# Optimization experiments

Measured on AMD Instinct MI355X. Metric: run time of the kernel, lower is better.

Reference implementation:

```python
import jax, jax.numpy as jnp
import numpy as np

CLAMP = 15  # relative positions clipped to [-15, 15], shifted to [0, 30]


def setup_inputs() -> dict:
    key = jax.random.key(0)
    ks = jax.random.split(key, 8)
    B, L, C, P = 2, 512, 256, 128
    return {
        "single_repr": jax.random.normal(ks[0], (B, L, C), jnp.float32),
        "pair_bias": jax.random.normal(ks[1], (B, L, L, 2), jnp.float32),
        "mask": jax.random.uniform(ks[2], (B, L), jnp.float32),
        "w_outer": jax.random.normal(ks[3], (C * C, P), jnp.float32) * (1.0 / C),
        "b_outer": jax.random.normal(ks[4], (P,), jnp.float32) * 0.02,
        "pos_embed": jax.random.normal(ks[5], (32, P), jnp.float32) * 0.02,
        "w_bias": jax.random.normal(ks[6], (2, P), jnp.float32) * 0.02,
        "b_bias": jax.random.normal(ks[7], (P,), jnp.float32) * 0.02,
    }


def reference(single_repr, pair_bias, mask, w_outer, b_outer, pos_embed, w_bias, b_bias):
    B, L, C = single_repr.shape
    P = w_outer.shape[-1]
    # Fused outer-product + projection: z[b,i,j,p] = sum_{c,d} s[b,i,c] s[b,j,d] W[c,d,p]
    # done as two matmuls, never materializing the [B,L,L,C,C] tensor.
    W = w_outer.reshape(C, C, P)
    tmp = jnp.einsum('bjd,cdp->bjcp', single_repr, W)          # [B,L,C,P]
    z = jnp.einsum('bic,bjcp->bijp', single_repr, tmp) + b_outer  # [B,L,L,P]
    # pair bias projection (pair_bias_dim=2 != pair_dim -> project)
    z = z + (pair_bias @ w_bias + b_bias)
    # relative-position embedding
    pos = jnp.arange(L)
    rel_pos = jnp.clip(pos[:, None] - pos[None, :], -CLAMP, CLAMP) + CLAMP  # [L,L] in [0,30]
    z = z + pos_embed[rel_pos]
    # pair mask
    pair_mask = mask[:, :, None] * mask[:, None, :]
    z = z * pair_mask[..., None]
    return z
```

## Files before the change

### kernel.cpp

```cpp
#include <hip/hip_runtime.h>
#include <stdint.h>

#define GLOBAL_AS __attribute__((address_space(1)))
#define LDS_AS    __attribute__((address_space(3)))

typedef __attribute__((ext_vector_type(8))) short short8;
typedef __attribute__((ext_vector_type(4))) float f32x4;
typedef __attribute__((ext_vector_type(4))) float float4v;
typedef __attribute__((ext_vector_type(4))) unsigned short ushort4v;

static constexpr int Bc = 2;
static constexpr int Lc = 512;
static constexpr int Cc = 256;
static constexpr int Pc = 128;
static constexpr int NP = Pc * Cc;

__device__ __forceinline__ unsigned short f2bf(float x) {
  unsigned int u = __builtin_bit_cast(unsigned int, x);
  u += 0x7FFFu + ((u >> 16) & 1u);
  return (unsigned short)(u >> 16);
}

__device__ __forceinline__ void gload_lds16(const void* g, void* l) {
  __builtin_amdgcn_global_load_lds((const GLOBAL_AS unsigned int*)g,
                                   (LDS_AS unsigned int*)l, 16, 0, 0);
}

__global__ void convert_s_kernel(const float* __restrict__ s,
                                 unsigned short* __restrict__ out) {
  const int idx = (blockIdx.x * 256 + threadIdx.x) * 4;
  float4v v = *(const float4v*)&s[idx];
  ushort4v o;
  #pragma unroll
  for (int i = 0; i < 4; ++i) o[i] = f2bf(v[i]);
  *(ushort4v*)&out[idx] = o;
}

__global__ void prep_w_kernel(const float* __restrict__ w,
                              unsigned short* __restrict__ wT) {
  __shared__ unsigned short lds[128 * 258];
  const int c = blockIdx.x;
  const int t = threadIdx.x;
  const float* wc = w + (size_t)c * (Cc * Pc);
  #pragma unroll 4
  for (int it = 0; it < 128; ++it) {
    const int idx = it * 256 + t;
    const int d = idx >> 7, p = idx & 127;
    lds[p * 258 + d] = f2bf(wc[idx]);
  }
  __syncthreads();
  unsigned short* o = wT + (size_t)c * NP;
  #pragma unroll 4
  for (int it = 0; it < 128; ++it) {
    const int idx = it * 256 + t;
    const int p = idx >> 8, d = idx & 255;
    o[idx] = lds[p * 258 + d];
  }
}

__global__ __launch_bounds__(256) void gemm1_kernel(
    const unsigned short* __restrict__ sbf,
    const unsigned short* __restrict__ wT,
    unsigned short* __restrict__ tmpT,
    int b) {
  __shared__ unsigned short As[128 * 64];
  __shared__ unsigned short Bs[128 * 64];
  const int tid = threadIdx.x;
  const int wave = tid >> 6, lane = tid & 63;
  const int n0 = blockIdx.x * 128;
  const int j0 = blockIdx.y * 128;
  const int p_wg = n0 >> 8;
  const int c_base = n0 & 255;
  const unsigned short* sA = sbf + b * Lc * Cc;

  const int wr = wave >> 1, wcn = wave & 1;
  const int lr = lane & 15, lk = (lane >> 4) << 3;

  f32x4 acc[4][4];
  const f32x4 zero = {0.f, 0.f, 0.f, 0.f};
  #pragma unroll
  for (int m = 0; m < 4; ++m)
    #pragma unroll
    for (int n = 0; n < 4; ++n) acc[m][n] = zero;

  #pragma unroll 1
  for (int kt = 0; kt < 4; ++kt) {
    const int d0 = kt * 64;
    __syncthreads();
    #pragma unroll
    for (int op = 0; op < 4; ++op) {
      const int idx = op * 256 + tid;
      const int row = idx >> 3, col = (idx & 7) << 3;
      gload_lds16(&sA[(j0 + row) * Cc + d0 + col],
                  &As[(size_t)(op * 256 + wave * 64) * 8]);
    }
    #pragma unroll
    for (int op = 0; op < 4; ++op) {
      const int idx = op * 256 + tid;
      const int row = idx >> 3, col = (idx & 7) << 3;
      gload_lds16(&wT[(size_t)(((c_base + row) << 7) + p_wg) * 256 + d0 + col],
                  &Bs[(size_t)(op * 256 + wave * 64) * 8]);
    }
    __syncthreads();
    #pragma unroll
    for (int kk = 0; kk < 2; ++kk) {
      short8 af[4], bfr[4];
      #pragma unroll
      for (int m = 0; m < 4; ++m)
        af[m] = *(const short8*)&As[(wr * 64 + m * 16 + lr) * 64 + kk * 32 + lk];
      #pragma unroll
      for (int n = 0; n < 4; ++n)
        bfr[n] = *(const short8*)&Bs[(wcn * 64 + n * 16 + lr) * 64 + kk * 32 + lk];
      #pragma unroll
      for (int m = 0; m < 4; ++m)
        #pragma unroll
        for (int n = 0; n < 4; ++n)
          acc[m][n] = __builtin_amdgcn_mfma_f32_16x16x32_bf16(af[m], bfr[n], acc[m][n], 0, 0, 0);
    }
  }

  const int rb = wr * 64 + ((lane >> 4) << 2);
  const int cb = wcn * 64 + lr;
  #pragma unroll
  for (int m = 0; m < 4; ++m)
    #pragma unroll
    for (int q = 0; q < 4; ++q) {
      const int row = rb + m * 16 + q;
      unsigned short* dst = &tmpT[(size_t)(j0 + row) * NP + n0 + cb];
      #pragma unroll
      for (int n = 0; n < 4; ++n) dst[n * 16] = f2bf(acc[m][n][q]);
    }
}

__global__ __launch_bounds__(256) void gemm2_kernel(
    const unsigned short* __restrict__ sbf,
    const unsigned short* __restrict__ tmpT,
    const float* __restrict__ pair_bias,
    const float* __restrict__ mask,
    const float* __restrict__ b_outer,
    const float* __restrict__ pos_embed,
    const float* __restrict__ w_bias,
    const float* __restrict__ b_bias,
    float* __restrict__ out,
    int b) {
  __shared__ unsigned short As[128 * 64];
  __shared__ unsigned short Bs[128 * 64];
  const int tid = threadIdx.x;
  const int wave = tid >> 6, lane = tid & 63;
  const int j = blockIdx.x;
  const int i0 = blockIdx.y * 128;
  const unsigned short* sA = sbf + b * Lc * Cc;
  const unsigned short* tB = tmpT + (size_t)j * NP;

  const int wr = wave >> 1, wcn = wave & 1;
  const int lr = lane & 15, lk = (lane >> 4) << 3;

  f32x4 acc[4][4];
  const f32x4 zero = {0.f, 0.f, 0.f, 0.f};
  #pragma unroll
  for (int m = 0; m < 4; ++m)
    #pragma unroll
    for (int n = 0; n < 4; ++n) acc[m][n] = zero;

  #pragma unroll 1
  for (int kt = 0; kt < 4; ++kt) {
    const int c0 = kt * 64;
    __syncthreads();
    #pragma unroll
    for (int op = 0; op < 4; ++op) {
      const int idx = op * 256 + tid;
      const int row = idx >> 3, col = (idx & 7) << 3;
      gload_lds16(&sA[(i0 + row) * Cc + c0 + col],
                  &As[(size_t)(op * 256 + wave * 64) * 8]);
    }
    #pragma unroll
    for (int op = 0; op < 4; ++op) {
      const int idx = op * 256 + tid;
      const int row = idx >> 3, col = (idx & 7) << 3;
      gload_lds16(&tB[row * 256 + c0 + col],
                  &Bs[(size_t)(op * 256 + wave * 64) * 8]);
    }
    __syncthreads();
    #pragma unroll
    for (int kk = 0; kk < 2; ++kk) {
      short8 af[4], bfr[4];
      #pragma unroll
      for (int m = 0; m < 4; ++m)
        af[m] = *(const short8*)&As[(wr * 64 + m * 16 + lr) * 64 + kk * 32 + lk];
      #pragma unroll
      for (int n = 0; n < 4; ++n)
        bfr[n] = *(const short8*)&Bs[(wcn * 64 + n * 16 + lr) * 64 + kk * 32 + lk];
      #pragma unroll
      for (int m = 0; m < 4; ++m)
        #pragma unroll
        for (int n = 0; n < 4; ++n)
          acc[m][n] = __builtin_amdgcn_mfma_f32_16x16x32_bf16(af[m], bfr[n], acc[m][n], 0, 0, 0);
    }
  }

  const int rb = wr * 64 + ((lane >> 4) << 2);
  const int cb = wcn * 64 + lr;
  const float mj = mask[b * Lc + j];
  #pragma unroll
  for (int m = 0; m < 4; ++m)
    #pragma unroll
    for (int q = 0; q < 4; ++q) {
      const int i = i0 + rb + m * 16 + q;
      const float mi = mask[b * Lc + i];
      const float sc = mi * mj;
      const size_t pbo = ((size_t)(b * Lc + i) * Lc + j) * 2;
      const float pb0 = pair_bias[pbo], pb1 = pair_bias[pbo + 1];
      int rel = i - j;
      rel = rel < -15 ? -15 : (rel > 15 ? 15 : rel);
      rel += 15;
      const float* pe = pos_embed + rel * Pc;
      float* dst = out + ((size_t)(b * Lc + i) * Lc + j) * Pc + cb;
      #pragma unroll
      for (int n = 0; n < 4; ++n) {
        const int p = cb + n * 16;
        float v = acc[m][n][q] + b_outer[p] + b_bias[p] +
                  pb0 * w_bias[p] + pb1 * w_bias[Pc + p] + pe[p];
        dst[n * 16] = v * sc;
      }
    }
}

extern "C" void kernel_launch(void* const* d_in, const int* in_sizes, int n_in,
                              void* d_out, int out_size, void* d_ws, size_t ws_size,
                              hipStream_t stream) {
  const float* s         = (const float*)d_in[0];
  const float* pair_bias = (const float*)d_in[1];
  const float* mask      = (const float*)d_in[2];
  const float* w_outer   = (const float*)d_in[3];
  const float* b_outer   = (const float*)d_in[4];
  const float* pos_embed = (const float*)d_in[5];
  const float* w_bias    = (const float*)d_in[6];
  const float* b_bias    = (const float*)d_in[7];
  float* out = (float*)d_out;

  unsigned char* ws = (unsigned char*)d_ws;
  unsigned short* s_bf = (unsigned short*)ws;
  unsigned short* wT   = (unsigned short*)(ws + (512u << 10));
  unsigned short* tmpT = (unsigned short*)(ws + (512u << 10) + (16u << 20));

  convert_s_kernel<<<256, 256, 0, stream>>>(s, s_bf);
  prep_w_kernel<<<256, 256, 0, stream>>>(w_outer, wT);

  for (int b = 0; b < Bc; ++b) {
    gemm1_kernel<<<dim3(256, 4), 256, 0, stream>>>(s_bf, wT, tmpT, b);
    gemm2_kernel<<<dim3(512, 4), 256, 0, stream>>>(s_bf, tmpT, pair_bias, mask,
                                                   b_outer, pos_embed, w_bias,
                                                   b_bias, out, b);
  }
}
```

Measured before the change: 452.2 us.

## Swap MFMA operand roles for vectorized epilogue stores and batch both batches per launch

```diff
diff --git a/kernel.cpp b/kernel.cpp
--- a/kernel.cpp
+++ b/kernel.cpp
@@ -7,6 +7,7 @@
 typedef __attribute__((ext_vector_type(8))) short short8;
 typedef __attribute__((ext_vector_type(4))) float f32x4;
 typedef __attribute__((ext_vector_type(4))) float float4v;
+typedef __attribute__((ext_vector_type(2))) float float2v;
 typedef __attribute__((ext_vector_type(4))) unsigned short ushort4v;
 
 static constexpr int Bc = 2;
@@ -14,6 +15,7 @@
 static constexpr int Cc = 256;
 static constexpr int Pc = 128;
 static constexpr int NP = Pc * Cc;
+static constexpr size_t TMPB = (size_t)Lc * NP;
 
 __device__ __forceinline__ unsigned short f2bf(float x) {
   unsigned int u = __builtin_bit_cast(unsigned int, x);
@@ -58,20 +60,23 @@
   }
 }
 
-__global__ __launch_bounds__(256) void gemm1_kernel(
+__global__ __launch_bounds__(256) void gemm1_swapped_kernel(
     const unsigned short* __restrict__ sbf,
     const unsigned short* __restrict__ wT,
     unsigned short* __restrict__ tmpT,
-    int b) {
-  __shared__ unsigned short As[128 * 64];
-  __shared__ unsigned short Bs[128 * 64];
+    int b_base) {
+  __shared__ unsigned short Ws[128 * 64];
+  __shared__ unsigned short Ss[128 * 64];
   const int tid = threadIdx.x;
   const int wave = tid >> 6, lane = tid & 63;
+  const int z = blockIdx.z;
+  const int b = b_base + z;
   const int n0 = blockIdx.x * 128;
   const int j0 = blockIdx.y * 128;
   const int p_wg = n0 >> 8;
   const int c_base = n0 & 255;
-  const unsigned short* sA = sbf + b * Lc * Cc;
+  const unsigned short* sB = sbf + b * Lc * Cc;
+  unsigned short* tT = tmpT + (size_t)z * TMPB;
 
   const int wr = wave >> 1, wcn = wave & 1;
   const int lr = lane & 15, lk = (lane >> 4) << 3;
@@ -91,48 +96,50 @@
     for (int op = 0; op < 4; ++op) {
       const int idx = op * 256 + tid;
       const int row = idx >> 3, col = (idx & 7) << 3;
-      gload_lds16(&sA[(j0 + row) * Cc + d0 + col],
-                  &As[(size_t)(op * 256 + wave * 64) * 8]);
-    }
-    #pragma unroll
-    for (int op = 0; op < 4; ++op) {
-      const int idx = op * 256 + tid;
-      const int row = idx >> 3, col = (idx & 7) << 3;
-      gload_lds16(&wT[(size_t)(((c_base + row) << 7) + p_wg) * 256 + d0 + col],
-                  &Bs[(size_t)(op * 256 + wave * 64) * 8]);
+      gload_lds16(&wT[(size_t)((c_base + row) * 128 + p_wg) * 256 + d0 + col],
+                  &Ws[(size_t)(op * 256 + wave * 64) * 8]);
+    }
+    #pragma unroll
+    for (int op = 0; op < 4; ++op) {
+      const int idx = op * 256 + tid;
+      const int row = idx >> 3, col = (idx & 7) << 3;
+      gload_lds16(&sB[(j0 + row) * Cc + d0 + col],
+                  &Ss[(size_t)(op * 256 + wave * 64) * 8]);
     }
     __syncthreads();
     #pragma unroll
     for (int kk = 0; kk < 2; ++kk) {
-      short8 af[4], bfr[4];
-      #pragma unroll
-      for (int m = 0; m < 4; ++m)
-        af[m] = *(const short8*)&As[(wr * 64 + m * 16 + lr) * 64 + kk * 32 + lk];
+      short8 aw[4], bs[4];
+      #pragma unroll
+      for (int m = 0; m < 4; ++m)
+        aw[m] = *(const short8*)&Ws[(wr * 64 + m * 16 + lr) * 64 + kk * 32 + lk];
       #pragma unroll
       for (int n = 0; n < 4; ++n)
-        bfr[n] = *(const short8*)&Bs[(wcn * 64 + n * 16 + lr) * 64 + kk * 32 + lk];
+        bs[n] = *(const short8*)&Ss[(wcn * 64 + n * 16 + lr) * 64 + kk * 32 + lk];
       #pragma unroll
       for (int m = 0; m < 4; ++m)
         #pragma unroll
         for (int n = 0; n < 4; ++n)
-          acc[m][n] = __builtin_amdgcn_mfma_f32_16x16x32_bf16(af[m], bfr[n], acc[m][n], 0, 0, 0);
-    }
-  }
-
-  const int rb = wr * 64 + ((lane >> 4) << 2);
-  const int cb = wcn * 64 + lr;
-  #pragma unroll
-  for (int m = 0; m < 4; ++m)
-    #pragma unroll
-    for (int q = 0; q < 4; ++q) {
-      const int row = rb + m * 16 + q;
-      unsigned short* dst = &tmpT[(size_t)(j0 + row) * NP + n0 + cb];
-      #pragma unroll
-      for (int n = 0; n < 4; ++n) dst[n * 16] = f2bf(acc[m][n][q]);
-    }
-}
-
-__global__ __launch_bounds__(256) void gemm2_kernel(
+          acc[m][n] = __builtin_amdgcn_mfma_f32_16x16x32_bf16(aw[m], bs[n], acc[m][n], 0, 0, 0);
+    }
+  }
+
+  const int rbase = wr * 64 + ((lane >> 4) << 2);
+  #pragma unroll
+  for (int n = 0; n < 4; ++n) {
+    const int j = j0 + wcn * 64 + n * 16 + lr;
+    unsigned short* dst = &tT[(size_t)j * NP + n0 + rbase];
+    #pragma unroll
+    for (int m = 0; m < 4; ++m) {
+      ushort4v o;
+      #pragma unroll
+      for (int q = 0; q < 4; ++q) o[q] = f2bf(acc[m][n][q]);
+      *(ushort4v*)&dst[m * 16] = o;
+    }
+  }
+}
+
+__global__ __launch_bounds__(256) void gemm2_swapped_kernel(
     const unsigned short* __restrict__ sbf,
     const unsigned short* __restrict__ tmpT,
     const float* __restrict__ pair_bias,
@@ -142,15 +149,17 @@
     const float* __restrict__ w_bias,
     const float* __restrict__ b_bias,
     float* __restrict__ out,
-    int b) {
-  __shared__ unsigned short As[128 * 64];
-  __shared__ unsigned short Bs[128 * 64];
+    int b_base) {
+  __shared__ unsigned short Ts[128 * 64];
+  __shared__ unsigned short Ss[128 * 64];
   const int tid = threadIdx.x;
   const int wave = tid >> 6, lane = tid & 63;
+  const int z = blockIdx.z;
+  const int b = b_base + z;
   const int j = blockIdx.x;
   const int i0 = blockIdx.y * 128;
-  const unsigned short* sA = sbf + b * Lc * Cc;
-  const unsigned short* tB = tmpT + (size_t)j * NP;
+  const unsigned short* sB = sbf + b * Lc * Cc;
+  const unsigned short* tB = tmpT + (size_t)z * TMPB + (size_t)j * NP;
 
   const int wr = wave >> 1, wcn = wave & 1;
   const int lr = lane & 15, lk = (lane >> 4) << 3;
@@ -170,59 +179,65 @@
     for (int op = 0; op < 4; ++op) {
       const int idx = op * 256 + tid;
       const int row = idx >> 3, col = (idx & 7) << 3;
-      gload_lds16(&sA[(i0 + row) * Cc + c0 + col],
-                  &As[(size_t)(op * 256 + wave * 64) * 8]);
-    }
-    #pragma unroll
-    for (int op = 0; op < 4; ++op) {
-      const int idx = op * 256 + tid;
-      const int row = idx >> 3, col = (idx & 7) << 3;
       gload_lds16(&tB[row * 256 + c0 + col],
-                  &Bs[(size_t)(op * 256 + wave * 64) * 8]);
+                  &Ts[(size_t)(op * 256 + wave * 64) * 8]);
+    }
+    #pragma unroll
+    for (int op = 0; op < 4; ++op) {
+      const int idx = op * 256 + tid;
+      const int row = idx >> 3, col = (idx & 7) << 3;
+      gload_lds16(&sB[(i0 + row) * Cc + c0 + col],
+                  &Ss[(size_t)(op * 256 + wave * 64) * 8]);
     }
     __syncthreads();
     #pragma unroll
     for (int kk = 0; kk < 2; ++kk) {
-      short8 af[4], bfr[4];
-      #pragma unroll
-      for (int m = 0; m < 4; ++m)
-        af[m] = *(const short8*)&As[(wr * 64 + m * 16 + lr) * 64 + kk * 32 + lk];
+      short8 at[4], bi[4];
+      #pragma unroll
+      for (int m = 0; m < 4; ++m)
+        at[m] = *(const short8*)&Ts[(wr * 64 + m * 16 + lr) * 64 + kk * 32 + lk];
       #pragma unroll
       for (int n = 0; n < 4; ++n)
-        bfr[n] = *(const short8*)&Bs[(wcn * 64 + n * 16 + lr) * 64 + kk * 32 + lk];
+        bi[n] = *(const short8*)&Ss[(wcn * 64 + n * 16 + lr) * 64 + kk * 32 + lk];
       #pragma unroll
       for (int m = 0; m < 4; ++m)
         #pragma unroll
         for (int n = 0; n < 4; ++n)
-          acc[m][n] = __builtin_amdgcn_mfma_f32_16x16x32_bf16(af[m], bfr[n], acc[m][n], 0, 0, 0);
-    }
-  }
-
-  const int rb = wr * 64 + ((lane >> 4) << 2);
-  const int cb = wcn * 64 + lr;
+          acc[m][n] = __builtin_amdgcn_mfma_f32_16x16x32_bf16(at[m], bi[n], acc[m][n], 0, 0, 0);
+    }
+  }
+
+  const int pbase = wr * 64 + ((lane >> 4) << 2);
   const float mj = mask[b * Lc + j];
-  #pragma unroll
-  for (int m = 0; m < 4; ++m)
-    #pragma unroll
-    for (int q = 0; q < 4; ++q) {
-      const int i = i0 + rb + m * 16 + q;
-      const float mi = mask[b * Lc + i];
-      const float sc = mi * mj;
-      const size_t pbo = ((size_t)(b * Lc + i) * Lc + j) * 2;
-      const float pb0 = pair_bias[pbo], pb1 = pair_bias[pbo + 1];
-      int rel = i - j;
-      rel = rel < -15 ? -15 : (rel > 15 ? 15 : rel);
-      rel += 15;
-      const float* pe = pos_embed + rel * Pc;
-      float* dst = out + ((size_t)(b * Lc + i) * Lc + j) * Pc + cb;
-      #pragma unroll
-      for (int n = 0; n < 4; ++n) {
-        const int p = cb + n * 16;
-        float v = acc[m][n][q] + b_outer[p] + b_bias[p] +
-                  pb0 * w_bias[p] + pb1 * w_bias[Pc + p] + pe[p];
-        dst[n * 16] = v * sc;
-      }
-    }
+
+  float4v bsum[4], wb0[4], wb1[4];
+  #pragma unroll
+  for (int m = 0; m < 4; ++m) {
+    const int p = pbase + m * 16;
+    bsum[m] = *(const float4v*)&b_outer[p] + *(const float4v*)&b_bias[p];
+    wb0[m] = *(const float4v*)&w_bias[p];
+    wb1[m] = *(const float4v*)&w_bias[Pc + p];
+  }
+
+  #pragma unroll
+  for (int n = 0; n < 4; ++n) {
+    const int i = i0 + wcn * 64 + n * 16 + lr;
+    const float sc = mask[b * Lc + i] * mj;
+    const size_t rowoff = (size_t)(b * Lc + i) * Lc + j;
+    const float2v pb = *(const float2v*)&pair_bias[rowoff * 2];
+    int rel = i - j;
+    rel = rel < -15 ? -15 : (rel > 15 ? 15 : rel);
+    rel += 15;
+    const float* pe_row = pos_embed + rel * Pc;
+    float* drow = out + rowoff * Pc;
+    #pragma unroll
+    for (int m = 0; m < 4; ++m) {
+      const int p = pbase + m * 16;
+      const float4v pe4 = *(const float4v*)&pe_row[p];
+      float4v v = acc[m][n] + bsum[m] + pb[0] * wb0[m] + pb[1] * wb1[m] + pe4;
+      *(float4v*)&drow[p] = v * sc;
+    }
+  }
 }
 
 extern "C" void kernel_launch(void* const* d_in, const int* in_sizes, int n_in,
@@ -243,13 +258,21 @@
   unsigned short* wT   = (unsigned short*)(ws + (512u << 10));
   unsigned short* tmpT = (unsigned short*)(ws + (512u << 10) + (16u << 20));
 
+  const size_t need_batched = (512u << 10) + (16u << 20) + 2 * (TMPB * 2);
+  const bool batched = ws_size >= need_batched;
+
   convert_s_kernel<<<256, 256, 0, stream>>>(s, s_bf);
   prep_w_kernel<<<256, 256, 0, stream>>>(w_outer, wT);
 
-  for (int b = 0; b < Bc; ++b) {
-    gemm1_kernel<<<dim3(256, 4), 256, 0, stream>>>(s_bf, wT, tmpT, b);
-    gemm2_kernel<<<dim3(512, 4), 256, 0, stream>>>(s_bf, tmpT, pair_bias, mask,
-                                                   b_outer, pos_embed, w_bias,
-                                                   b_bias, out, b);
-  }
-}
+  if (batched) {
+    gemm1_swapped_kernel<<<dim3(256, 4, 2), 256, 0, stream>>>(s_bf, wT, tmpT, 0);
+    gemm2_swapped_kernel<<<dim3(512, 4, 2), 256, 0, stream>>>(
+        s_bf, tmpT, pair_bias, mask, b_outer, pos_embed, w_bias, b_bias, out, 0);
+  } else {
+    for (int b = 0; b < Bc; ++b) {
+      gemm1_swapped_kernel<<<dim3(256, 4, 1), 256, 0, stream>>>(s_bf, wT, tmpT, b);
+      gemm2_swapped_kernel<<<dim3(512, 4, 1), 256, 0, stream>>>(
+          s_bf, tmpT, pair_bias, mask, b_outer, pos_embed, w_bias, b_bias, out, b);
+    }
+  }
+}
```

Result: faster. 438.1 us (-3.1%).
